# Optimization experiments

Hardware: AMD Instinct MI355X
Metric: run time of the kernel (lower is better)

## Reference

```python
import jax, jax.numpy as jnp
import numpy as np

LA, LB, D = 4096, 4096, 1024

def setup_inputs() -> dict:
    key = jax.random.key(0)
    ka, kb = jax.random.split(key)
    a_hat = jax.random.normal(ka, (LA, D), dtype=jnp.float32)
    b_hat = jax.random.normal(kb, (LB, D), dtype=jnp.float32)
    return {"a_hat": a_hat, "b_hat": b_hat}

def _m_vector(v_hat, v_wave):
    # concat along dim 0, matching torch.concat(..., dim=0)
    return jnp.concatenate((v_hat, v_wave, v_hat - v_wave, v_hat * v_wave), axis=0)

def reference(a_hat, b_hat):
    # energy: [La, Lb]
    energy = jnp.matmul(a_hat, b_hat.T)
    # softmax over columns (dim 1) -> attend over b rows
    wave_a = jnp.matmul(jax.nn.softmax(energy, axis=1), b_hat)      # [La, D]
    # softmax over rows (dim 0), transposed -> attend over a rows
    wave_b = jnp.matmul(jax.nn.softmax(energy, axis=0).T, a_hat)    # [Lb, D]
    m_a = _m_vector(a_hat, wave_a)   # [4*La, D]
    m_b = _m_vector(b_hat, wave_b)   # [4*Lb, D]
    return (m_a, m_b)
```

## Files before the change

kernel.cpp:

```cpp
#include <hip/hip_runtime.h>
#include <cstdint>
#include <cstddef>

#define LA 4096
#define LB 4096
#define DD 1024

typedef unsigned short u16;
typedef short bf16x8 __attribute__((ext_vector_type(8)));
typedef float f32x4 __attribute__((ext_vector_type(4)));

__device__ __forceinline__ u16 f2bf(float f) {
  unsigned u = __builtin_bit_cast(unsigned, f);
  u += 0x7fffu + ((u >> 16) & 1u);
  return (u16)(u >> 16);
}
__device__ __forceinline__ float bf2f(u16 h) {
  return __builtin_bit_cast(float, (unsigned)h << 16);
}
__device__ __forceinline__ bf16x8 pack8(float4 a, float4 b) {
  bf16x8 r;
  r[0] = (short)f2bf(a.x); r[1] = (short)f2bf(a.y);
  r[2] = (short)f2bf(a.z); r[3] = (short)f2bf(a.w);
  r[4] = (short)f2bf(b.x); r[5] = (short)f2bf(b.y);
  r[6] = (short)f2bf(b.z); r[7] = (short)f2bf(b.w);
  return r;
}
__device__ __forceinline__ void async16(const void* g, void* l) {
  __builtin_amdgcn_global_load_lds(
      (const __attribute__((address_space(1))) unsigned int*)g,
      (__attribute__((address_space(3))) unsigned int*)l, 16, 0, 0);
}

__global__ __launch_bounds__(256) void split_ab(const float* __restrict__ A,
                                                const float* __restrict__ B,
                                                u16* __restrict__ Ahi, u16* __restrict__ Alo,
                                                u16* __restrict__ Bhi, u16* __restrict__ Blo) {
  const int side = blockIdx.x >> 11;
  const size_t idx = ((size_t)(blockIdx.x & 2047) * 256 + threadIdx.x) * 8;
  const float* src = side ? B : A;
  u16* dh = side ? Bhi : Ahi;
  u16* dl = side ? Blo : Alo;
  const float4 a = *(const float4*)&src[idx];
  const float4 b = *(const float4*)&src[idx + 4];
  float v[8] = {a.x, a.y, a.z, a.w, b.x, b.y, b.z, b.w};
  bf16x8 hi, lo;
#pragma unroll
  for (int i = 0; i < 8; ++i) {
    const u16 h = f2bf(v[i]);
    hi[i] = (short)h;
    lo[i] = (short)f2bf(v[i] - bf2f(h));
  }
  *(bf16x8*)&dh[idx] = hi;
  *(bf16x8*)&dl[idx] = lo;
}

__global__ __launch_bounds__(256) void tr_f32(const float* __restrict__ in,
                                              u16* __restrict__ out,
                                              int R, int C) {
  __shared__ u16 t[32][33];
  const int c0 = blockIdx.x * 32, r0 = blockIdx.y * 32;
  const int tid = threadIdx.x;
  const int lr = tid >> 3, lc = (tid & 7) * 4;
  const float4 v = *(const float4*)&in[(size_t)(r0 + lr) * C + c0 + lc];
  t[lr][lc + 0] = f2bf(v.x); t[lr][lc + 1] = f2bf(v.y);
  t[lr][lc + 2] = f2bf(v.z); t[lr][lc + 3] = f2bf(v.w);
  __syncthreads();
  ushort4 w;
  w.x = t[lc + 0][lr]; w.y = t[lc + 1][lr]; w.z = t[lc + 2][lr]; w.w = t[lc + 3][lr];
  *(ushort4*)&out[(size_t)(c0 + lr) * R + r0 + lc] = w;
}

__global__ __launch_bounds__(256) void gemm_energy(const u16* __restrict__ Ahi,
                                                   const u16* __restrict__ Alo,
                                                   const u16* __restrict__ Bhi,
                                                   const u16* __restrict__ Blo,
                                                   float* __restrict__ E) {
  __shared__ u16 lah[128 * 32], lal[128 * 32], lbh[128 * 32], lbl[128 * 32];
  const int j0 = blockIdx.x * 128;
  const int i0 = blockIdx.y * 128;
  const int tid = threadIdx.x;
  const int lane = tid & 63, quad = lane >> 4, lq = lane & 15;
  const int wave = tid >> 6;
  const int wm = (wave & 1) * 64, wn = (wave >> 1) * 64;
  f32x4 acc[4][4] = {};
  for (int kt = 0; kt < DD; kt += 32) {
    if (kt) __syncthreads();
#pragma unroll
    for (int r = 0; r < 2; ++r) {
      const int chunk = wave * 128 + r * 64 + lane;
      const int row = chunk >> 2;
      const int kc = (chunk & 3) * 8;
      const int lofs = (wave * 128 + r * 64) * 16;
      const size_t ga = (size_t)(i0 + row) * DD + kt + kc;
      const size_t gb = (size_t)(j0 + row) * DD + kt + kc;
      async16(Ahi + ga, (char*)lah + lofs);
      async16(Alo + ga, (char*)lal + lofs);
      async16(Bhi + gb, (char*)lbh + lofs);
      async16(Blo + gb, (char*)lbl + lofs);
    }
    __syncthreads();
    bf16x8 fah[4], fal[4], fbh[4], fbl[4];
#pragma unroll
    for (int f = 0; f < 4; ++f) {
      fah[f] = *(const bf16x8*)&lah[(wm + f * 16 + lq) * 32 + quad * 8];
      fal[f] = *(const bf16x8*)&lal[(wm + f * 16 + lq) * 32 + quad * 8];
      fbh[f] = *(const bf16x8*)&lbh[(wn + f * 16 + lq) * 32 + quad * 8];
      fbl[f] = *(const bf16x8*)&lbl[(wn + f * 16 + lq) * 32 + quad * 8];
    }
#pragma unroll
    for (int fm = 0; fm < 4; ++fm)
#pragma unroll
      for (int fn = 0; fn < 4; ++fn) {
        acc[fm][fn] = __builtin_amdgcn_mfma_f32_16x16x32_bf16(fal[fm], fbh[fn], acc[fm][fn], 0, 0, 0);
        acc[fm][fn] = __builtin_amdgcn_mfma_f32_16x16x32_bf16(fah[fm], fbl[fn], acc[fm][fn], 0, 0, 0);
        acc[fm][fn] = __builtin_amdgcn_mfma_f32_16x16x32_bf16(fah[fm], fbh[fn], acc[fm][fn], 0, 0, 0);
      }
  }
#pragma unroll
  for (int fm = 0; fm < 4; ++fm)
#pragma unroll
    for (int fn = 0; fn < 4; ++fn)
#pragma unroll
      for (int r = 0; r < 4; ++r) {
        const int gi = i0 + wm + fm * 16 + quad * 4 + r;
        const int gj = j0 + wn + fn * 16 + lq;
        E[(size_t)gi * LB + gj] = acc[fm][fn][r];
      }
}

__global__ __launch_bounds__(256) void row_stats(const float* __restrict__ E,
                                                 float* __restrict__ rmax,
                                                 float* __restrict__ rinv) {
  __shared__ float red[8];
  const int row = blockIdx.x, tid = threadIdx.x;
  const float* e = E + (size_t)row * LB;
  float4 v[4];
#pragma unroll
  for (int c = 0; c < 4; ++c) v[c] = *(const float4*)&e[(c * 256 + tid) * 4];
  float m = -__builtin_inff();
#pragma unroll
  for (int c = 0; c < 4; ++c)
    m = fmaxf(m, fmaxf(fmaxf(v[c].x, v[c].y), fmaxf(v[c].z, v[c].w)));
#pragma unroll
  for (int o = 32; o > 0; o >>= 1) m = fmaxf(m, __shfl_down(m, o));
  if ((tid & 63) == 0) red[tid >> 6] = m;
  __syncthreads();
  m = fmaxf(fmaxf(red[0], red[1]), fmaxf(red[2], red[3]));
  float s = 0.f;
#pragma unroll
  for (int c = 0; c < 4; ++c)
    s += __expf(v[c].x - m) + __expf(v[c].y - m) + __expf(v[c].z - m) + __expf(v[c].w - m);
#pragma unroll
  for (int o = 32; o > 0; o >>= 1) s += __shfl_down(s, o);
  if ((tid & 63) == 0) red[4 + (tid >> 6)] = s;
  __syncthreads();
  if (tid == 0) {
    rmax[row] = m;
    rinv[row] = 1.f / (red[4] + red[5] + red[6] + red[7]);
  }
}

__global__ __launch_bounds__(256) void col_partial(const float* __restrict__ E,
                                                   float* __restrict__ pmax,
                                                   float* __restrict__ psum) {
  const int c = blockIdx.x * 256 + threadIdx.x;
  const int rg = blockIdx.y;
  const float* e = E + (size_t)rg * 128 * LB + c;
  float m = -__builtin_inff(), s = 0.f;
#pragma unroll 4
  for (int r = 0; r < 128; ++r) {
    const float x = e[(size_t)r * LB];
    const float nm = fmaxf(m, x);
    s = s * __expf(m - nm) + __expf(x - nm);
    m = nm;
  }
  pmax[rg * LB + c] = m;
  psum[rg * LB + c] = s;
}

__global__ __launch_bounds__(256) void col_combine(const float* __restrict__ pmax,
                                                   const float* __restrict__ psum,
                                                   float* __restrict__ cmax,
                                                   float* __restrict__ cinv) {
  const int c = blockIdx.x * 256 + threadIdx.x;
  float m = -__builtin_inff(), s = 0.f;
#pragma unroll 4
  for (int g = 0; g < 32; ++g) {
    const float pm = pmax[g * LB + c], ps = psum[g * LB + c];
    const float nm = fmaxf(m, pm);
    s = s * __expf(m - nm) + ps * __expf(pm - nm);
    m = nm;
  }
  cmax[c] = m;
  cinv[c] = 1.f / s;
}

__global__ __launch_bounds__(256) void make_pa(const float* __restrict__ E,
                                               const float* __restrict__ rmax,
                                               u16* __restrict__ P) {
  const int i = blockIdx.x;
  const int c = threadIdx.x * 16;
  const float* e = E + (size_t)i * LB + c;
  const float rm = rmax[i];
  const float4 x0 = *(const float4*)(e);
  const float4 x1 = *(const float4*)(e + 4);
  const float4 x2 = *(const float4*)(e + 8);
  const float4 x3 = *(const float4*)(e + 12);
  float4 y0, y1, y2, y3;
  y0.x = __expf(x0.x - rm); y0.y = __expf(x0.y - rm); y0.z = __expf(x0.z - rm); y0.w = __expf(x0.w - rm);
  y1.x = __expf(x1.x - rm); y1.y = __expf(x1.y - rm); y1.z = __expf(x1.z - rm); y1.w = __expf(x1.w - rm);
  y2.x = __expf(x2.x - rm); y2.y = __expf(x2.y - rm); y2.z = __expf(x2.z - rm); y2.w = __expf(x2.w - rm);
  y3.x = __expf(x3.x - rm); y3.y = __expf(x3.y - rm); y3.z = __expf(x3.z - rm); y3.w = __expf(x3.w - rm);
  *(bf16x8*)&P[(size_t)i * LB + c] = pack8(y0, y1);
  *(bf16x8*)&P[(size_t)i * LB + c + 8] = pack8(y2, y3);
}

__global__ __launch_bounds__(256) void make_pb(const float* __restrict__ E,
                                               const float* __restrict__ cmax,
                                               u16* __restrict__ P) {
  __shared__ u16 t[32][33];
  const int j0 = blockIdx.x * 32;
  const int i0 = blockIdx.y * 32;
  const int tid = threadIdx.x;
  const int lr = tid >> 3, lc = (tid & 7) * 4;
  const float4 v = *(const float4*)&E[(size_t)(i0 + lr) * LB + j0 + lc];
  const float4 cm = *(const float4*)&cmax[j0 + lc];
  t[lr][lc + 0] = f2bf(__expf(v.x - cm.x));
  t[lr][lc + 1] = f2bf(__expf(v.y - cm.y));
  t[lr][lc + 2] = f2bf(__expf(v.z - cm.z));
  t[lr][lc + 3] = f2bf(__expf(v.w - cm.w));
  __syncthreads();
  ushort4 w;
  w.x = t[lc + 0][lr]; w.y = t[lc + 1][lr]; w.z = t[lc + 2][lr]; w.w = t[lc + 3][lr];
  *(ushort4*)&P[(size_t)(j0 + lr) * LA + i0 + lc] = w;
}

__global__ __launch_bounds__(256) void gemm_pv(const u16* __restrict__ P,
                                               const u16* __restrict__ Vt,
                                               const float* __restrict__ inv,
                                               float* __restrict__ W) {
  __shared__ u16 lds_a[128 * 32];
  __shared__ u16 lds_b[128 * 32];
  const int n0 = blockIdx.x * 128;
  const int i0 = blockIdx.y * 128;
  const int tid = threadIdx.x;
  const int lane = tid & 63, quad = lane >> 4, lq = lane & 15;
  const int wave = tid >> 6;
  const int wm = (wave & 1) * 64, wn = (wave >> 1) * 64;
  f32x4 acc[4][4] = {};
  for (int kt = 0; kt < 4096; kt += 32) {
    if (kt) __syncthreads();
#pragma unroll
    for (int r = 0; r < 2; ++r) {
      const int chunk = wave * 128 + r * 64 + lane;
      const int row = chunk >> 2;
      const int kc = (chunk & 3) * 8;
      const int lofs = (wave * 128 + r * 64) * 16;
      async16(P + (size_t)(i0 + row) * 4096 + kt + kc, (char*)lds_a + lofs);
      async16(Vt + (size_t)(n0 + row) * 4096 + kt + kc, (char*)lds_b + lofs);
    }
    __syncthreads();
    bf16x8 af[4], bfr[4];
#pragma unroll
    for (int f = 0; f < 4; ++f) {
      af[f]  = *(const bf16x8*)&lds_a[(wm + f * 16 + lq) * 32 + quad * 8];
      bfr[f] = *(const bf16x8*)&lds_b[(wn + f * 16 + lq) * 32 + quad * 8];
    }
#pragma unroll
    for (int fm = 0; fm < 4; ++fm)
#pragma unroll
      for (int fn = 0; fn < 4; ++fn)
        acc[fm][fn] = __builtin_amdgcn_mfma_f32_16x16x32_bf16(af[fm], bfr[fn], acc[fm][fn], 0, 0, 0);
  }
#pragma unroll
  for (int fm = 0; fm < 4; ++fm)
#pragma unroll
    for (int r = 0; r < 4; ++r) {
      const int gm = i0 + wm + fm * 16 + quad * 4 + r;
      const float sc = inv[gm];
#pragma unroll
      for (int fn = 0; fn < 4; ++fn) {
        const int gn = n0 + wn + fn * 16 + lq;
        W[(size_t)gm * DD + gn] = acc[fm][fn][r] * sc;
      }
    }
}

__global__ __launch_bounds__(256) void finish(const float* __restrict__ Ain,
                                              const float* __restrict__ Bin,
                                              float* __restrict__ out) {
  const int side = blockIdx.x >> 11;
  const int blk = blockIdx.x & 2047;
  const size_t idx = ((size_t)blk * 256 + threadIdx.x) * 8;
  const size_t S = (size_t)LA * DD;
  const float* src = side ? Bin : Ain;
  float* ob = out + (size_t)side * 4 * S;
  const float4 a0 = *(const float4*)&src[idx];
  const float4 a1 = *(const float4*)&src[idx + 4];
  const float4 w0 = *(const float4*)&ob[S + idx];
  const float4 w1 = *(const float4*)&ob[S + idx + 4];
  float4 s0, s1, m0, m1;
  s0.x = a0.x - w0.x; s0.y = a0.y - w0.y; s0.z = a0.z - w0.z; s0.w = a0.w - w0.w;
  s1.x = a1.x - w1.x; s1.y = a1.y - w1.y; s1.z = a1.z - w1.z; s1.w = a1.w - w1.w;
  m0.x = a0.x * w0.x; m0.y = a0.y * w0.y; m0.z = a0.z * w0.z; m0.w = a0.w * w0.w;
  m1.x = a1.x * w1.x; m1.y = a1.y * w1.y; m1.z = a1.z * w1.z; m1.w = a1.w * w1.w;
  *(float4*)&ob[idx] = a0;            *(float4*)&ob[idx + 4] = a1;
  *(float4*)&ob[2 * S + idx] = s0;    *(float4*)&ob[2 * S + idx + 4] = s1;
  *(float4*)&ob[3 * S + idx] = m0;    *(float4*)&ob[3 * S + idx + 4] = m1;
}

extern "C" void kernel_launch(void* const* d_in, const int* in_sizes, int n_in,
                              void* d_out, int out_size, void* d_ws, size_t ws_size,
                              hipStream_t stream) {
  const float* A = (const float*)d_in[0];
  const float* B = (const float*)d_in[1];
  float* out = (float*)d_out;
  const size_t S = (size_t)LA * DD;

  float* pmax = out;
  float* psum = pmax + 131072;
  float* rmax = psum + 131072;
  float* rinv = rmax + 4096;
  float* cmax = rinv + 4096;
  float* cinv = cmax + 4096;
  u16*   Bt   = (u16*)(out + 1048576);
  u16*   Ahi  = (u16*)(out + 2 * S);
  u16*   Alo  = Ahi + S;
  u16*   Bhi  = Alo + S;
  u16*   Blo  = Bhi + S;
  u16*   P    = (u16*)(out + 2 * S);
  float* E    = out + 4 * S;
  u16*   At   = (u16*)(out + 4 * S);
  float* wave_a = out + S;
  float* wave_b = out + 5 * S;

  split_ab<<<dim3(4096), 256, 0, stream>>>(A, B, Ahi, Alo, Bhi, Blo);
  gemm_energy<<<dim3(LB / 128, LA / 128), 256, 0, stream>>>(Ahi, Alo, Bhi, Blo, E);
  row_stats<<<dim3(LA), 256, 0, stream>>>(E, rmax, rinv);
  col_partial<<<dim3(LB / 256, 32), 256, 0, stream>>>(E, pmax, psum);
  col_combine<<<dim3(LB / 256), 256, 0, stream>>>(pmax, psum, cmax, cinv);

  tr_f32<<<dim3(DD / 32, LB / 32), 256, 0, stream>>>(B, Bt, LB, DD);
  make_pa<<<dim3(LA), 256, 0, stream>>>(E, rmax, P);
  gemm_pv<<<dim3(DD / 128, LA / 128), 256, 0, stream>>>(P, Bt, rinv, wave_a);

  make_pb<<<dim3(LB / 32, LA / 32), 256, 0, stream>>>(E, cmax, P);
  tr_f32<<<dim3(DD / 32, LA / 32), 256, 0, stream>>>(A, At, LA, DD);
  gemm_pv<<<dim3(DD / 128, LB / 128), 256, 0, stream>>>(P, At, cinv, wave_b);

  finish<<<dim3(4096), 256, 0, stream>>>(A, B, out);
}
```

Measured before the change: 504.0 us.

## Fuse row softmax exp into stats kernel and split-K the PV GEMMs

Row statistics and the exponentiated bf16 P matrix are now produced in one pass over each energy row, removing a separate make_pa read of E. Both P·V GEMMs are split along K into two halves to double block count and fill more CUs. The wave_a side combines halves with float atomics into a pre-zeroed output, and the wave_b side writes a partial buffer that the finish kernel adds. Atomics add nondeterministic summation order and extra memory traffic for partials.

Measured after the change: 466.4 us. 1.08x faster.

```diff
diff --git a/kernel.cpp b/kernel.cpp
--- a/kernel.cpp
+++ b/kernel.cpp
@@ -129,9 +129,10 @@
       }
 }
 
-__global__ __launch_bounds__(256) void row_stats(const float* __restrict__ E,
-                                                 float* __restrict__ rmax,
-                                                 float* __restrict__ rinv) {
+__global__ __launch_bounds__(256) void row_softmax_pa(const float* __restrict__ E,
+                                                      float* __restrict__ rinv,
+                                                      u16* __restrict__ P,
+                                                      float* __restrict__ wa) {
   __shared__ float red[8];
   const int row = blockIdx.x, tid = threadIdx.x;
   const float* e = E + (size_t)row * LB;
@@ -155,10 +156,18 @@
   for (int o = 32; o > 0; o >>= 1) s += __shfl_down(s, o);
   if ((tid & 63) == 0) red[4 + (tid >> 6)] = s;
   __syncthreads();
-  if (tid == 0) {
-    rmax[row] = m;
-    rinv[row] = 1.f / (red[4] + red[5] + red[6] + red[7]);
-  }
+  if (tid == 0) rinv[row] = 1.f / (red[4] + red[5] + red[6] + red[7]);
+#pragma unroll
+  for (int c = 0; c < 4; ++c) {
+    ushort4 w;
+    w.x = f2bf(__expf(v[c].x - m));
+    w.y = f2bf(__expf(v[c].y - m));
+    w.z = f2bf(__expf(v[c].z - m));
+    w.w = f2bf(__expf(v[c].w - m));
+    *(ushort4*)&P[(size_t)row * LB + (c * 256 + tid) * 4] = w;
+  }
+  float4 z = {0.f, 0.f, 0.f, 0.f};
+  *(float4*)&wa[(size_t)row * DD + tid * 4] = z;
 }
 
 __global__ __launch_bounds__(256) void col_partial(const float* __restrict__ E,
@@ -194,26 +203,6 @@
   }
   cmax[c] = m;
   cinv[c] = 1.f / s;
-}
-
-__global__ __launch_bounds__(256) void make_pa(const float* __restrict__ E,
-                                               const float* __restrict__ rmax,
-                                               u16* __restrict__ P) {
-  const int i = blockIdx.x;
-  const int c = threadIdx.x * 16;
-  const float* e = E + (size_t)i * LB + c;
-  const float rm = rmax[i];
-  const float4 x0 = *(const float4*)(e);
-  const float4 x1 = *(const float4*)(e + 4);
-  const float4 x2 = *(const float4*)(e + 8);
-  const float4 x3 = *(const float4*)(e + 12);
-  float4 y0, y1, y2, y3;
-  y0.x = __expf(x0.x - rm); y0.y = __expf(x0.y - rm); y0.z = __expf(x0.z - rm); y0.w = __expf(x0.w - rm);
-  y1.x = __expf(x1.x - rm); y1.y = __expf(x1.y - rm); y1.z = __expf(x1.z - rm); y1.w = __expf(x1.w - rm);
-  y2.x = __expf(x2.x - rm); y2.y = __expf(x2.y - rm); y2.z = __expf(x2.z - rm); y2.w = __expf(x2.w - rm);
-  y3.x = __expf(x3.x - rm); y3.y = __expf(x3.y - rm); y3.z = __expf(x3.z - rm); y3.w = __expf(x3.w - rm);
-  *(bf16x8*)&P[(size_t)i * LB + c] = pack8(y0, y1);
-  *(bf16x8*)&P[(size_t)i * LB + c + 8] = pack8(y2, y3);
 }
 
 __global__ __launch_bounds__(256) void make_pb(const float* __restrict__ E,
@@ -236,21 +225,25 @@
   *(ushort4*)&P[(size_t)(j0 + lr) * LA + i0 + lc] = w;
 }
 
+template <int ATOMIC>
 __global__ __launch_bounds__(256) void gemm_pv(const u16* __restrict__ P,
                                                const u16* __restrict__ Vt,
                                                const float* __restrict__ inv,
-                                               float* __restrict__ W) {
+                                               float* __restrict__ W0,
+                                               float* __restrict__ W1) {
   __shared__ u16 lds_a[128 * 32];
   __shared__ u16 lds_b[128 * 32];
   const int n0 = blockIdx.x * 128;
   const int i0 = blockIdx.y * 128;
+  const int kz = blockIdx.z;
   const int tid = threadIdx.x;
   const int lane = tid & 63, quad = lane >> 4, lq = lane & 15;
   const int wave = tid >> 6;
   const int wm = (wave & 1) * 64, wn = (wave >> 1) * 64;
   f32x4 acc[4][4] = {};
-  for (int kt = 0; kt < 4096; kt += 32) {
-    if (kt) __syncthreads();
+  for (int t = 0; t < 64; ++t) {
+    const int kt = kz * 2048 + t * 32;
+    if (t) __syncthreads();
 #pragma unroll
     for (int r = 0; r < 2; ++r) {
       const int chunk = wave * 128 + r * 64 + lane;
@@ -273,6 +266,7 @@
       for (int fn = 0; fn < 4; ++fn)
         acc[fm][fn] = __builtin_amdgcn_mfma_f32_16x16x32_bf16(af[fm], bfr[fn], acc[fm][fn], 0, 0, 0);
   }
+  float* W = ATOMIC ? W0 : (kz ? W1 : W0);
 #pragma unroll
   for (int fm = 0; fm < 4; ++fm)
 #pragma unroll
@@ -282,13 +276,17 @@
 #pragma unroll
       for (int fn = 0; fn < 4; ++fn) {
         const int gn = n0 + wn + fn * 16 + lq;
-        W[(size_t)gm * DD + gn] = acc[fm][fn][r] * sc;
+        if (ATOMIC)
+          unsafeAtomicAdd(&W[(size_t)gm * DD + gn], acc[fm][fn][r] * sc);
+        else
+          W[(size_t)gm * DD + gn] = acc[fm][fn][r] * sc;
       }
     }
 }
 
 __global__ __launch_bounds__(256) void finish(const float* __restrict__ Ain,
                                               const float* __restrict__ Bin,
+                                              const float* __restrict__ p1,
                                               float* __restrict__ out) {
   const int side = blockIdx.x >> 11;
   const int blk = blockIdx.x & 2047;
@@ -298,8 +296,16 @@
   float* ob = out + (size_t)side * 4 * S;
   const float4 a0 = *(const float4*)&src[idx];
   const float4 a1 = *(const float4*)&src[idx + 4];
-  const float4 w0 = *(const float4*)&ob[S + idx];
-  const float4 w1 = *(const float4*)&ob[S + idx + 4];
+  float4 w0 = *(const float4*)&ob[S + idx];
+  float4 w1 = *(const float4*)&ob[S + idx + 4];
+  if (side) {
+    const float4 q0 = *(const float4*)&p1[idx];
+    const float4 q1 = *(const float4*)&p1[idx + 4];
+    w0.x += q0.x; w0.y += q0.y; w0.z += q0.z; w0.w += q0.w;
+    w1.x += q1.x; w1.y += q1.y; w1.z += q1.z; w1.w += q1.w;
+    *(float4*)&ob[S + idx] = w0;
+    *(float4*)&ob[S + idx + 4] = w1;
+  }
   float4 s0, s1, m0, m1;
   s0.x = a0.x - w0.x; s0.y = a0.y - w0.y; s0.z = a0.z - w0.z; s0.w = a0.w - w0.w;
   s1.x = a1.x - w1.x; s1.y = a1.y - w1.y; s1.z = a1.z - w1.z; s1.w = a1.w - w1.w;
@@ -334,20 +340,21 @@
   u16*   At   = (u16*)(out + 4 * S);
   float* wave_a = out + S;
   float* wave_b = out + 5 * S;
+  float* pB1    = out + 6 * S;
 
   split_ab<<<dim3(4096), 256, 0, stream>>>(A, B, Ahi, Alo, Bhi, Blo);
   gemm_energy<<<dim3(LB / 128, LA / 128), 256, 0, stream>>>(Ahi, Alo, Bhi, Blo, E);
-  row_stats<<<dim3(LA), 256, 0, stream>>>(E, rmax, rinv);
+
+  row_softmax_pa<<<dim3(LA), 256, 0, stream>>>(E, rinv, P, wave_a);
   col_partial<<<dim3(LB / 256, 32), 256, 0, stream>>>(E, pmax, psum);
   col_combine<<<dim3(LB / 256), 256, 0, stream>>>(pmax, psum, cmax, cinv);
 
   tr_f32<<<dim3(DD / 32, LB / 32), 256, 0, stream>>>(B, Bt, LB, DD);
-  make_pa<<<dim3(LA), 256, 0, stream>>>(E, rmax, P);
-  gemm_pv<<<dim3(DD / 128, LA / 128), 256, 0, stream>>>(P, Bt, rinv, wave_a);
+  gemm_pv<1><<<dim3(DD / 128, LA / 128, 2), 256, 0, stream>>>(P, Bt, rinv, wave_a, nullptr);
 
   make_pb<<<dim3(LB / 32, LA / 32), 256, 0, stream>>>(E, cmax, P);
   tr_f32<<<dim3(DD / 32, LA / 32), 256, 0, stream>>>(A, At, LA, DD);
-  gemm_pv<<<dim3(DD / 128, LB / 128), 256, 0, stream>>>(P, At, cinv, wave_b);
-
-  finish<<<dim3(4096), 256, 0, stream>>>(A, B, out);
-}
+  gemm_pv<0><<<dim3(DD / 128, LB / 128, 2), 256, 0, stream>>>(P, At, cinv, wave_b, pB1);
+
+  finish<<<dim3(4096), 256, 0, stream>>>(A, B, pB1, out);
+}
```
